# Performance work log

Measured on AMD Instinct MI355X. Metric: run time of the kernel, lower is better.

Reference implementation:

```python
import jax, jax.numpy as jnp
import numpy as np

N = 100000      # nodes
E = 1600000     # edges
F_IN = 64       # num_node_features
R = 8           # num_relations
G = 256         # graphs in batch
H, C = 4, 32    # GAT heads, per-head channels
NEG_SLOPE_ATT = 0.2    # GATConv attention leaky relu
NEG_SLOPE = 0.01       # F.leaky_relu default


def setup_inputs() -> dict:
    key = jax.random.key(0)
    ks = jax.random.split(key, 12)
    init = lambda k, shape, fan: (jax.random.normal(k, shape, jnp.float32) / np.sqrt(fan).astype(np.float32))
    x = jax.random.normal(ks[0], (N, F_IN), jnp.float32)
    edge_index = jax.random.randint(ks[1], (2, E), 0, N)
    edge_type = jax.random.randint(ks[2], (E,), 0, R)
    batch = (jnp.arange(N) * G) // N  # sorted graph ids, every segment non-empty
    return dict(
        x=x, edge_index=edge_index, edge_type=edge_type, batch=batch,
        gat_w=init(ks[3], (F_IN, H * C), F_IN),
        gat_att_src=init(ks[4], (H, C), C),
        gat_att_dst=init(ks[5], (H, C), C),
        gat_bias=jnp.zeros((H * C,), jnp.float32),
        dense1_w=init(ks[6], (H * C, 16), H * C),
        dense1_b=jnp.zeros((16,), jnp.float32),
        rw1=init(ks[7], (R, F_IN, 32), F_IN),
        root1=init(ks[8], (F_IN, 32), F_IN),
        rb1=jnp.zeros((32,), jnp.float32),
        rw2=init(ks[9], (R, 32, 16), 32),
        root2=init(ks[10], (32, 16), 32),
        rb2=jnp.zeros((16,), jnp.float32),
        dense_w=init(ks[11], (32, 1), 32),
        dense_b=jnp.zeros((1,), jnp.float32),
    )


def _gat(x, src, dst, w, att_src, att_dst, bias):
    h = (x @ w).reshape(N, H, C)                       # [N,H,C]
    a_src = jnp.sum(h * att_src, axis=-1)              # [N,H]
    a_dst = jnp.sum(h * att_dst, axis=-1)              # [N,H]
    e = jax.nn.leaky_relu(a_src[src] + a_dst[dst], NEG_SLOPE_ATT)  # [E,H]
    # segment softmax over incoming edges of each dst node
    m = jax.ops.segment_max(e, dst, num_segments=N)    # [N,H]
    p = jnp.exp(e - m[dst])
    s = jax.ops.segment_sum(p, dst, num_segments=N)    # [N,H]
    alpha = p / s[dst]
    msg = h[src] * alpha[:, :, None]                   # [E,H,C]
    out = jax.ops.segment_sum(msg, dst, num_segments=N)
    return out.reshape(N, H * C) + bias


def _rgcn(x, src, dst, edge_type, w, root, bias):
    # per-relation transform of all nodes, then edge gather (PyG RGCNConv, aggr='mean')
    xw = jnp.einsum('ni,rio->rno', x, w)               # [R,N,out]
    msg = xw[edge_type, src]                           # [E,out]
    comb = dst * R + edge_type                         # mean is per (dst, relation)
    cnt = jax.ops.segment_sum(jnp.ones((E,), x.dtype), comb, num_segments=N * R)
    agg = jax.ops.segment_sum(msg / cnt[comb][:, None], dst, num_segments=N)
    return agg + x @ root + bias


def reference(x, edge_index, edge_type, batch, gat_w, gat_att_src, gat_att_dst,
              gat_bias, dense1_w, dense1_b, rw1, root1, rb1, rw2, root2, rb2,
              dense_w, dense_b):
    src, dst = edge_index[0], edge_index[1]
    # GAT branch (dropout treated as identity / eval mode)
    h = _gat(x, src, dst, gat_w, gat_att_src, gat_att_dst, gat_bias)
    h = jax.nn.leaky_relu(h, NEG_SLOPE)
    h = jax.nn.leaky_relu(h @ dense1_w + dense1_b, NEG_SLOPE)
    gmax = jax.ops.segment_max(h, batch, num_segments=G)          # [G,16]
    # RGCN branch
    z = jax.nn.relu(_rgcn(x, src, dst, edge_type, rw1, root1, rb1))
    z = jax.nn.relu(_rgcn(z, src, dst, edge_type, rw2, root2, rb2))
    nodes_per_graph = jax.ops.segment_sum(jnp.ones((N,), x.dtype), batch, num_segments=G)
    gmean = jax.ops.segment_sum(z, batch, num_segments=G) / nodes_per_graph[:, None]
    # fuse
    zc = jnp.concatenate([gmax, gmean], axis=1)                   # [G,32]
    return zc @ dense_w + dense_b                                  # [G,1]
```

## Files before the change

### kernel.cpp

```cpp
#include <hip/hip_runtime.h>
#include <hip/hip_bf16.h>

typedef __hip_bfloat16 bf16;
typedef unsigned short u16;

#define N_NODES 100000
#define N_EDGES 1600000
#define F_IN 64
#define N_REL 8
#define N_GRAPH 256
#define N_HEAD 4
#define HC 128
#define NBLK_SCAN 391

__device__ __forceinline__ float lrelu(float x, float s) { return x >= 0.f ? x : s * x; }
__device__ __forceinline__ unsigned fenc(float f) {
  unsigned b = __float_as_uint(f);
  return (b & 0x80000000u) ? ~b : (b | 0x80000000u);
}
__device__ __forceinline__ float fdec(unsigned u) {
  float v = __uint_as_float((u & 0x80000000u) ? (u & 0x7fffffffu) : ~u);
  return fmaxf(fminf(v, 3e38f), -3e38f);
}
__device__ __forceinline__ float bf2f(bf16 v) { return __bfloat162float(v); }
__device__ __forceinline__ bf16 f2bf(float v) { return __float2bfloat16(v); }
__device__ __forceinline__ float lo_bf(unsigned u) { return __uint_as_float(u << 16); }
__device__ __forceinline__ float hi_bf(unsigned u) { return __uint_as_float(u & 0xFFFF0000u); }
__device__ __forceinline__ unsigned f2bfu(float v) {
  unsigned u = __float_as_uint(v);
  return (u + 0x7FFFu + ((u >> 16) & 1u)) >> 16;
}

template<bool BF> __device__ __forceinline__ float ldf(const void* p, size_t i) {
  if (BF) { u16 v = ((const u16*)p)[i]; return __uint_as_float(((unsigned)v) << 16); }
  else    { return ((const float*)p)[i]; }
}

__global__ void k_probe(const u16* __restrict__ xr, int* __restrict__ flag) {
  int t = threadIdx.x;
  int c = 0;
  for (int i = t; i < 1024; i += 256) {
    unsigned e = (xr[i] >> 7) & 0xFFu;
    if (e >= 100u && e <= 140u) c++;
  }
  __shared__ int sc[256];
  sc[t] = c;
  __syncthreads();
  for (int s = 128; s; s >>= 1) { if (t < s) sc[t] += sc[t + s]; __syncthreads(); }
  if (t == 0) *flag = (sc[0] >= 800) ? 1 : 0;
}

template<bool BF>
__device__ __forceinline__ void gat_h_body(const void* x, const void* w, const void* att_s,
                                           const void* att_d, u16* __restrict__ h,
                                           float* __restrict__ a_src, float* __restrict__ a_dst) {
  int n = blockIdx.x, j = threadIdx.x;
  __shared__ float xs[F_IN];
  if (j < F_IN) xs[j] = ldf<BF>(x, (size_t)n * F_IN + j);
  __syncthreads();
  float acc = 0.f;
#pragma unroll
  for (int k = 0; k < F_IN; ++k) acc += xs[k] * ldf<BF>(w, (size_t)k * HC + j);
  h[(size_t)n * HC + j] = (u16)f2bfu(acc);
  float ps = acc * ldf<BF>(att_s, j);
  float pd = acc * ldf<BF>(att_d, j);
#pragma unroll
  for (int off = 16; off > 0; off >>= 1) {
    ps += __shfl_down(ps, off, 32);
    pd += __shfl_down(pd, off, 32);
  }
  if ((j & 31) == 0) {
    a_src[n * N_HEAD + (j >> 5)] = ps;
    a_dst[n * N_HEAD + (j >> 5)] = pd;
  }
}
__global__ void k_gat_h(const void* x, const void* w, const void* att_s, const void* att_d,
                        u16* h, float* a_src, float* a_dst, const int* flag) {
  if (__builtin_amdgcn_readfirstlane(*flag)) gat_h_body<true>(x, w, att_s, att_d, h, a_src, a_dst);
  else gat_h_body<false>(x, w, att_s, att_d, h, a_src, a_dst);
}

__global__ void k_hist(const int* __restrict__ ei, const int* __restrict__ etype,
                       int* __restrict__ deg, int* __restrict__ cnt) {
  int e = blockIdx.x * 256 + threadIdx.x;
  if (e >= N_EDGES) return;
  int d = ei[N_EDGES + e], t = etype[e];
  atomicAdd(&deg[d], 1);
  atomicAdd(&cnt[d * N_REL + t], 1);
}

__global__ void k_scan_a(const int* __restrict__ deg, int* __restrict__ rowptr,
                         int* __restrict__ scanblk) {
  __shared__ int buf[256];
  int tid = threadIdx.x;
  int i = blockIdx.x * 256 + tid;
  int v = (i < N_NODES) ? deg[i] : 0;
  buf[tid] = v;
  __syncthreads();
  for (int st = 1; st < 256; st <<= 1) {
    int t = buf[tid];
    int a = (tid >= st) ? buf[tid - st] : 0;
    __syncthreads();
    buf[tid] = t + a;
    __syncthreads();
  }
  if (i < N_NODES) rowptr[i] = buf[tid] - v;
  if (tid == 255) scanblk[blockIdx.x] = buf[255];
}
__global__ void k_scan_b(int* __restrict__ scanblk) {
  __shared__ int buf[512];
  int tid = threadIdx.x;
  int v = (tid < NBLK_SCAN) ? scanblk[tid] : 0;
  buf[tid] = v;
  __syncthreads();
  for (int st = 1; st < 512; st <<= 1) {
    int t = buf[tid];
    int a = (tid >= st) ? buf[tid - st] : 0;
    __syncthreads();
    buf[tid] = t + a;
    __syncthreads();
  }
  if (tid < NBLK_SCAN) scanblk[tid] = buf[tid] - v;
}
__global__ void k_scan_c(int* __restrict__ rowptr, int* __restrict__ wp,
                         const int* __restrict__ scanblk) {
  int i = blockIdx.x * 256 + threadIdx.x;
  if (i < N_NODES) {
    int val = rowptr[i] + scanblk[blockIdx.x];
    rowptr[i] = val;
    wp[i] = val;
  } else if (i == N_NODES) {
    rowptr[N_NODES] = N_EDGES;
  }
}

__global__ void k_scatter(const int* __restrict__ ei, const int* __restrict__ etype,
                          const float* __restrict__ a_src, const float* __restrict__ a_dst,
                          int* __restrict__ wp, unsigned* __restrict__ csr,
                          float4* __restrict__ p_logit, int* __restrict__ dstarr) {
  int e = blockIdx.x * 256 + threadIdx.x;
  if (e >= N_EDGES) return;
  int sn = ei[e], d = ei[N_EDGES + e], t = etype[e];
  int pos = atomicAdd(&wp[d], 1);
  csr[pos] = (unsigned)sn | ((unsigned)t << 20);
  dstarr[pos] = d;
  const float4 as = *(const float4*)&a_src[sn * 4];
  const float4 ad = *(const float4*)&a_dst[d * 4];
  float4 lg;
  lg.x = lrelu(as.x + ad.x, 0.2f);
  lg.y = lrelu(as.y + ad.y, 0.2f);
  lg.z = lrelu(as.z + ad.z, 0.2f);
  lg.w = lrelu(as.w + ad.w, 0.2f);
  p_logit[pos] = lg;
}

__global__ void k_msum(const int* __restrict__ rowptr, const float* __restrict__ p_logit,
                       float* __restrict__ m_arr, float* __restrict__ si_arr) {
  int tid = threadIdx.x;
  int n = blockIdx.x * 16 + (tid >> 4);
  int l16 = tid & 15, head = l16 & 3, slot = l16 >> 2;
  int base = rowptr[n], deg = rowptr[n + 1] - base;
  float m = -1e30f;
  for (int i = slot; i < deg; i += 4) m = fmaxf(m, p_logit[(size_t)(base + i) * 4 + head]);
  m = fmaxf(m, __shfl_xor(m, 4, 64));
  m = fmaxf(m, __shfl_xor(m, 8, 64));
  float s = 0.f;
  for (int i = slot; i < deg; i += 4) s += __expf(p_logit[(size_t)(base + i) * 4 + head] - m);
  s += __shfl_xor(s, 4, 64);
  s += __shfl_xor(s, 8, 64);
  if (slot == 0) {
    m_arr[n * 4 + head] = m;
    si_arr[n * 4 + head] = (deg > 0) ? 1.f / s : 0.f;
  }
}

__global__ void k_alpha(const int* __restrict__ dstarr, const float* __restrict__ m_arr,
                        const float* __restrict__ si_arr, float4* __restrict__ plog4) {
  int p = blockIdx.x * 256 + threadIdx.x;
  if (p >= N_EDGES) return;
  int d = dstarr[p];
  float4 lg = plog4[p];
  const float4 m4 = *(const float4*)&m_arr[d * 4];
  const float4 s4 = *(const float4*)&si_arr[d * 4];
  float4 a;
  a.x = __expf(lg.x - m4.x) * s4.x;
  a.y = __expf(lg.y - m4.y) * s4.y;
  a.z = __expf(lg.z - m4.z) * s4.z;
  a.w = __expf(lg.w - m4.w) * s4.w;
  plog4[p] = a;
}

template<bool BF>
__device__ __forceinline__ void gat_agg_body(const int* __restrict__ rowptr,
                                             const unsigned* __restrict__ csr,
                                             const float* __restrict__ alpha,
                                             const uint2* __restrict__ hu2, const void* gbias,
                                             const void* d1w, const void* d1b,
                                             const int* __restrict__ batch,
                                             unsigned* __restrict__ gmax, int* __restrict__ npg) {
  int tid = threadIdx.x;
  int wave = tid >> 6, l = tid & 63;
  int d = blockIdx.x * 4 + wave;
  __shared__ float os[4][132];
  int base = rowptr[d];
  int deg = rowptr[d + 1] - base;
  int slot = l >> 5, cl = l & 31;
  int head = cl >> 3;
  float a0 = 0.f, a1 = 0.f, a2 = 0.f, a3 = 0.f;
  int i = slot;
  for (; i + 6 < deg; i += 8) {
    unsigned sp0 = csr[base + i],     sp1 = csr[base + i + 2];
    unsigned sp2 = csr[base + i + 4], sp3 = csr[base + i + 6];
    float av0 = alpha[(size_t)(base + i) * 4 + head];
    float av1 = alpha[(size_t)(base + i + 2) * 4 + head];
    float av2 = alpha[(size_t)(base + i + 4) * 4 + head];
    float av3 = alpha[(size_t)(base + i + 6) * 4 + head];
    uint2 h0 = hu2[(size_t)(sp0 & 0xFFFFF) * 32 + cl];
    uint2 h1 = hu2[(size_t)(sp1 & 0xFFFFF) * 32 + cl];
    uint2 h2 = hu2[(size_t)(sp2 & 0xFFFFF) * 32 + cl];
    uint2 h3 = hu2[(size_t)(sp3 & 0xFFFFF) * 32 + cl];
    a0 += lo_bf(h0.x) * av0 + lo_bf(h1.x) * av1 + lo_bf(h2.x) * av2 + lo_bf(h3.x) * av3;
    a1 += hi_bf(h0.x) * av0 + hi_bf(h1.x) * av1 + hi_bf(h2.x) * av2 + hi_bf(h3.x) * av3;
    a2 += lo_bf(h0.y) * av0 + lo_bf(h1.y) * av1 + lo_bf(h2.y) * av2 + lo_bf(h3.y) * av3;
    a3 += hi_bf(h0.y) * av0 + hi_bf(h1.y) * av1 + hi_bf(h2.y) * av2 + hi_bf(h3.y) * av3;
  }
  for (; i < deg; i += 2) {
    unsigned sp = csr[base + i];
    float av = alpha[(size_t)(base + i) * 4 + head];
    uint2 hv = hu2[(size_t)(sp & 0xFFFFF) * 32 + cl];
    a0 += lo_bf(hv.x) * av;
    a1 += hi_bf(hv.x) * av;
    a2 += lo_bf(hv.y) * av;
    a3 += hi_bf(hv.y) * av;
  }
  a0 += __shfl_xor(a0, 32, 64);
  a1 += __shfl_xor(a1, 32, 64);
  a2 += __shfl_xor(a2, 32, 64);
  a3 += __shfl_xor(a3, 32, 64);
  if (slot == 0) {
    os[wave][4 * cl + 0] = lrelu(a0 + ldf<BF>(gbias, 4 * cl + 0), 0.01f);
    os[wave][4 * cl + 1] = lrelu(a1 + ldf<BF>(gbias, 4 * cl + 1), 0.01f);
    os[wave][4 * cl + 2] = lrelu(a2 + ldf<BF>(gbias, 4 * cl + 2), 0.01f);
    os[wave][4 * cl + 3] = lrelu(a3 + ldf<BF>(gbias, 4 * cl + 3), 0.01f);
  }
  __syncthreads();
  if (tid < 64) {
    int node = tid >> 4, out = tid & 15;
    float acc = ldf<BF>(d1b, out);
#pragma unroll
    for (int k = 0; k < HC; ++k) acc += os[node][k] * ldf<BF>(d1w, (size_t)k * 16 + out);
    acc = lrelu(acc, 0.01f);
    atomicMax(&gmax[batch[blockIdx.x * 4 + node] * 16 + out], fenc(acc));
  }
  if (tid < 4) atomicAdd(&npg[batch[blockIdx.x * 4 + tid]], 1);
}
__global__ void k_gat_agg(const int* rowptr, const unsigned* csr, const float* alpha,
                          const u16* h, const void* gbias, const void* d1w, const void* d1b,
                          const int* batch, unsigned* gmax, int* npg, const int* flag) {
  if (__builtin_amdgcn_readfirstlane(*flag))
    gat_agg_body<true>(rowptr, csr, alpha, (const uint2*)h, gbias, d1w, d1b, batch, gmax, npg);
  else
    gat_agg_body<false>(rowptr, csr, alpha, (const uint2*)h, gbias, d1w, d1b, batch, gmax, npg);
}

template<bool BF>
__device__ __forceinline__ void xw1_body(const void* x, const void* rw1, bf16* __restrict__ xw1) {
  __shared__ float xs[8][F_IN];
  int tid = threadIdx.x;
  int n0 = blockIdx.x * 8;
  for (int i = tid; i < 8 * F_IN; i += 256) {
    int nn = n0 + (i >> 6);
    xs[i >> 6][i & 63] = (nn < N_NODES) ? ldf<BF>(x, (size_t)nn * F_IN + (i & 63)) : 0.f;
  }
  __syncthreads();
  int nl = tid >> 5, c = tid & 31;
  int n = n0 + nl, r = blockIdx.y;
  float acc = 0.f;
#pragma unroll
  for (int k = 0; k < F_IN; ++k) acc += xs[nl][k] * ldf<BF>(rw1, (size_t)(r * F_IN + k) * 32 + c);
  if (n < N_NODES) xw1[((size_t)r * N_NODES + n) * 32 + c] = f2bf(acc);
}
__global__ void k_xw1(const void* x, const void* rw1, bf16* xw1, const int* flag) {
  if (__builtin_amdgcn_readfirstlane(*flag)) xw1_body<true>(x, rw1, xw1);
  else xw1_body<false>(x, rw1, xw1);
}

template<bool BF>
__device__ __forceinline__ void ragg1_body(const int* __restrict__ rowptr,
                                           const unsigned* __restrict__ csr,
                                           const int* __restrict__ cnt,
                                           const u16* __restrict__ xw, const void* x,
                                           const void* root1, const void* rb1,
                                           float* __restrict__ z1) {
  __shared__ float xs[4][F_IN];
  __shared__ float cinv[4][N_REL];
  int tid = threadIdx.x;
  int n0 = blockIdx.x * 4;
  {
    int nn = n0 + (tid >> 6);
    xs[tid >> 6][tid & 63] = ldf<BF>(x, (size_t)nn * F_IN + (tid & 63));
  }
  if (tid < 32) {
    int cv = cnt[(n0 + (tid >> 3)) * N_REL + (tid & 7)];
    cinv[tid >> 3][tid & 7] = (cv > 0) ? 1.f / (float)cv : 0.f;
  }
  __syncthreads();
  int wave = tid >> 6, l = tid & 63;
  int half = l >> 5, c = l & 31;
  int n = n0 + wave;
  int base = rowptr[n], deg = rowptr[n + 1] - base;
  float acc = 0.f;
  int i = half;
  for (; i + 2 < deg; i += 4) {
    unsigned sp0 = csr[base + i], sp1 = csr[base + i + 2];
    int t0 = sp0 >> 20, t1 = sp1 >> 20;
    u16 v0 = xw[((size_t)t0 * N_NODES + (sp0 & 0xFFFFF)) * 32 + c];
    u16 v1 = xw[((size_t)t1 * N_NODES + (sp1 & 0xFFFFF)) * 32 + c];
    acc += __uint_as_float(((unsigned)v0) << 16) * cinv[wave][t0];
    acc += __uint_as_float(((unsigned)v1) << 16) * cinv[wave][t1];
  }
  if (i < deg) {
    unsigned sp = csr[base + i];
    int t = sp >> 20;
    u16 v = xw[((size_t)t * N_NODES + (sp & 0xFFFFF)) * 32 + c];
    acc += __uint_as_float(((unsigned)v) << 16) * cinv[wave][t];
  }
  float r = 0.f;
#pragma unroll
  for (int kk = 0; kk < 32; ++kk) {
    int k = half * 32 + kk;
    r += xs[wave][k] * ldf<BF>(root1, (size_t)k * 32 + c);
  }
  float tot = acc + r;
  tot += __shfl_xor(tot, 32, 64);
  if (half == 0) z1[(size_t)n * 32 + c] = fmaxf(tot + ldf<BF>(rb1, c), 0.f);
}
__global__ void k_ragg1(const int* rowptr, const unsigned* csr, const int* cnt,
                        const bf16* xw1, const void* x, const void* root1, const void* rb1,
                        float* z1, const int* flag) {
  if (__builtin_amdgcn_readfirstlane(*flag))
    ragg1_body<true>(rowptr, csr, cnt, (const u16*)xw1, x, root1, rb1, z1);
  else
    ragg1_body<false>(rowptr, csr, cnt, (const u16*)xw1, x, root1, rb1, z1);
}

template<bool BF>
__device__ __forceinline__ void zw2_body(const float* __restrict__ z1, const void* rw2,
                                         bf16* __restrict__ zw2) {
  __shared__ float zs[16][32];
  int tid = threadIdx.x;
  int n0 = blockIdx.x * 16;
  for (int i = tid; i < 16 * 32; i += 256) {
    int nn = n0 + (i >> 5);
    zs[i >> 5][i & 31] = (nn < N_NODES) ? z1[(size_t)nn * 32 + (i & 31)] : 0.f;
  }
  __syncthreads();
  int nl = tid >> 4, c = tid & 15;
  int n = n0 + nl, r = blockIdx.y;
  float acc = 0.f;
#pragma unroll
  for (int k = 0; k < 32; ++k) acc += zs[nl][k] * ldf<BF>(rw2, (size_t)(r * 32 + k) * 16 + c);
  if (n < N_NODES) zw2[((size_t)r * N_NODES + n) * 16 + c] = f2bf(acc);
}
__global__ void k_zw2(const float* z1, const void* rw2, bf16* zw2, const int* flag) {
  if (__builtin_amdgcn_readfirstlane(*flag)) zw2_body<true>(z1, rw2, zw2);
  else zw2_body<false>(z1, rw2, zw2);
}

template<bool BF>
__device__ __forceinline__ void ragg2_body(const int* __restrict__ rowptr,
                                           const unsigned* __restrict__ csr,
                                           const int* __restrict__ cnt,
                                           const u16* __restrict__ zw,
                                           const float* __restrict__ z1, const void* root2,
                                           const void* rb2, const int* __restrict__ batch,
                                           float* __restrict__ gsum) {
  __shared__ float zs[4][33];
  __shared__ float cinv[4][N_REL];
  int tid = threadIdx.x;
  int n0 = blockIdx.x * 4;
  if (tid < 128) {
    int nn = n0 + (tid >> 5);
    zs[tid >> 5][tid & 31] = z1[(size_t)nn * 32 + (tid & 31)];
  }
  if (tid < 32) {
    int cv = cnt[(n0 + (tid >> 3)) * N_REL + (tid & 7)];
    cinv[tid >> 3][tid & 7] = (cv > 0) ? 1.f / (float)cv : 0.f;
  }
  __syncthreads();
  int wave = tid >> 6, l = tid & 63;
  int q = l >> 4, c = l & 15;
  int n = n0 + wave;
  int base = rowptr[n], deg = rowptr[n + 1] - base;
  float acc = 0.f;
  int i = q;
  for (; i + 4 < deg; i += 8) {
    unsigned sp0 = csr[base + i], sp1 = csr[base + i + 4];
    int t0 = sp0 >> 20, t1 = sp1 >> 20;
    u16 v0 = zw[((size_t)t0 * N_NODES + (sp0 & 0xFFFFF)) * 16 + c];
    u16 v1 = zw[((size_t)t1 * N_NODES + (sp1 & 0xFFFFF)) * 16 + c];
    acc += __uint_as_float(((unsigned)v0) << 16) * cinv[wave][t0];
    acc += __uint_as_float(((unsigned)v1) << 16) * cinv[wave][t1];
  }
  if (i < deg) {
    unsigned sp = csr[base + i];
    int t = sp >> 20;
    u16 v = zw[((size_t)t * N_NODES + (sp & 0xFFFFF)) * 16 + c];
    acc += __uint_as_float(((unsigned)v) << 16) * cinv[wave][t];
  }
  float r = 0.f;
#pragma unroll
  for (int kk = 0; kk < 8; ++kk) {
    int k = q * 8 + kk;
    r += zs[wave][k] * ldf<BF>(root2, (size_t)k * 16 + c);
  }
  float tot = acc + r;
  tot += __shfl_xor(tot, 16, 64);
  tot += __shfl_xor(tot, 32, 64);
  if (q == 0) {
    float z2 = fmaxf(tot + ldf<BF>(rb2, c), 0.f);
    atomicAdd(&gsum[batch[n] * 16 + c], z2);
  }
}
__global__ void k_ragg2(const int* rowptr, const unsigned* csr, const int* cnt,
                        const bf16* zw2, const float* z1, const void* root2, const void* rb2,
                        const int* batch, float* gsum, const int* flag) {
  if (__builtin_amdgcn_readfirstlane(*flag))
    ragg2_body<true>(rowptr, csr, cnt, (const u16*)zw2, z1, root2, rb2, batch, gsum);
  else
    ragg2_body<false>(rowptr, csr, cnt, (const u16*)zw2, z1, root2, rb2, batch, gsum);
}

template<bool BF>
__device__ __forceinline__ void final_body(const unsigned* __restrict__ gmax,
                                           const float* __restrict__ gsum,
                                           const int* __restrict__ npg, const void* dw,
                                           const void* db, void* out) {
  int g = threadIdx.x;
  if (g >= N_GRAPH) return;
  float acc = ldf<BF>(db, 0);
  int np = npg[g]; if (np < 1) np = 1;
  float inv = 1.f / (float)np;
#pragma unroll
  for (int c = 0; c < 16; ++c) {
    acc += fdec(gmax[g * 16 + c]) * ldf<BF>(dw, c);
    acc += (gsum[g * 16 + c] * inv) * ldf<BF>(dw, 16 + c);
  }
  if (BF) ((bf16*)out)[g] = f2bf(acc);
  else ((float*)out)[g] = acc;
}
__global__ void k_final(const unsigned* gmax, const float* gsum, const int* npg,
                        const void* dw, const void* db, void* out, const int* flag) {
  if (__builtin_amdgcn_readfirstlane(*flag)) final_body<true>(gmax, gsum, npg, dw, db, out);
  else final_body<false>(gmax, gsum, npg, dw, db, out);
}

extern "C" void kernel_launch(void* const* d_in, const int* in_sizes, int n_in,
                              void* d_out, int out_size, void* d_ws, size_t ws_size,
                              hipStream_t stream) {
  const void* x        = d_in[0];
  const int*  ei       = (const int*)d_in[1];
  const int*  etype    = (const int*)d_in[2];
  const int*  batch    = (const int*)d_in[3];
  const void* gat_w    = d_in[4];
  const void* att_src  = d_in[5];
  const void* att_dst  = d_in[6];
  const void* gat_bias = d_in[7];
  const void* d1w      = d_in[8];
  const void* d1b      = d_in[9];
  const void* rw1      = d_in[10];
  const void* root1    = d_in[11];
  const void* rb1      = d_in[12];
  const void* rw2      = d_in[13];
  const void* root2    = d_in[14];
  const void* rb2      = d_in[15];
  const void* dw       = d_in[16];
  const void* db       = d_in[17];

  char* ws = (char*)d_ws;
  const size_t o_h     = 0;
  const size_t o_plog  = 25600000;
  const size_t o_xw1   = 0;
  const size_t o_zw2   = 0;
  const size_t o_asrc  = 51200000;
  const size_t o_adst  = 52800000;
  const size_t o_deg   = 54400000;
  const size_t o_rowp  = 54800000;
  const size_t o_wp    = 55200016;
  const size_t o_cnt   = 55600032;
  const size_t o_csr   = 58800032;
  const size_t o_z1    = 65200032;
  const size_t o_sblk  = 78000032;
  const size_t o_gmax  = 78001600;
  const size_t o_gsum  = 78017984;
  const size_t o_npg   = 78034368;
  const size_t o_flag  = 78035392;
  const size_t o_dst   = 78035400;
  const size_t total   = 84435400;
  if (ws_size < total) return;

  u16*      h      = (u16*)(ws + o_h);
  float*    plog   = (float*)(ws + o_plog);
  bf16*     xw1    = (bf16*)(ws + o_xw1);
  bf16*     zw2    = (bf16*)(ws + o_zw2);
  float*    a_src  = (float*)(ws + o_asrc);
  float*    a_dst  = (float*)(ws + o_adst);
  int*      deg    = (int*)(ws + o_deg);
  int*      rowptr = (int*)(ws + o_rowp);
  int*      wp     = (int*)(ws + o_wp);
  int*      cnt    = (int*)(ws + o_cnt);
  unsigned* csr    = (unsigned*)(ws + o_csr);
  float*    z1     = (float*)(ws + o_z1);
  int*      sblk   = (int*)(ws + o_sblk);
  unsigned* gmax   = (unsigned*)(ws + o_gmax);
  float*    gsum   = (float*)(ws + o_gsum);
  int*      npg    = (int*)(ws + o_npg);
  int*      flag   = (int*)(ws + o_flag);
  int*      dstarr = (int*)(ws + o_dst);

  k_probe<<<1, 256, 0, stream>>>((const u16*)x, flag);

  hipMemsetAsync(ws + o_deg, 0, o_csr - o_deg, stream);
  hipMemsetAsync(ws + o_gmax, 0, 33792, stream);

  k_gat_h<<<N_NODES, 128, 0, stream>>>(x, gat_w, att_src, att_dst, h, a_src, a_dst, flag);

  k_hist<<<(N_EDGES + 255) / 256, 256, 0, stream>>>(ei, etype, deg, cnt);
  k_scan_a<<<NBLK_SCAN, 256, 0, stream>>>(deg, rowptr, sblk);
  k_scan_b<<<1, 512, 0, stream>>>(sblk);
  k_scan_c<<<NBLK_SCAN, 256, 0, stream>>>(rowptr, wp, sblk);
  k_scatter<<<(N_EDGES + 255) / 256, 256, 0, stream>>>(ei, etype, a_src, a_dst, wp, csr,
                                                       (float4*)plog, dstarr);

  k_msum<<<N_NODES / 16, 256, 0, stream>>>(rowptr, plog, a_src, a_dst);
  k_alpha<<<(N_EDGES + 255) / 256, 256, 0, stream>>>(dstarr, a_src, a_dst, (float4*)plog);

  k_gat_agg<<<N_NODES / 4, 256, 0, stream>>>(rowptr, csr, plog, h, gat_bias, d1w, d1b, batch,
                                             gmax, npg, flag);

  k_xw1<<<dim3((N_NODES + 7) / 8, N_REL), 256, 0, stream>>>(x, rw1, xw1, flag);
  k_ragg1<<<N_NODES / 4, 256, 0, stream>>>(rowptr, csr, cnt, xw1, x, root1, rb1, z1, flag);

  k_zw2<<<dim3((N_NODES + 15) / 16, N_REL), 256, 0, stream>>>(z1, rw2, zw2, flag);
  k_ragg2<<<N_NODES / 4, 256, 0, stream>>>(rowptr, csr, cnt, zw2, z1, root2, rb2,
                                           batch, gsum, flag);

  k_final<<<1, 256, 0, stream>>>(gmax, gsum, npg, dw, db, d_out, flag);
}
```

Measured before the change: 1.231 ms.

## Aggregate raw features per relation before transform, fuse GAT projection with histogram

RGCN layers no longer precompute per-relation transformed features (xw1, zw2) for all nodes. Instead each destination node sums raw bf16 neighbour features per relation in registers and then applies the relation weights once per node, using the linearity of the mean aggregation. This removes two large precompute kernels and their scattered gathers, at the cost of an 8-way per-relation accumulator, more registers, and a small per-node matmul. The GAT projection kernel and the degree histogram are merged into one launch, and bf16 copies of x and z1 are written for the gathers.

```diff
diff --git a/kernel.cpp b/kernel.cpp
--- a/kernel.cpp
+++ b/kernel.cpp
@@ -22,10 +22,9 @@
   float v = __uint_as_float((u & 0x80000000u) ? (u & 0x7fffffffu) : ~u);
   return fmaxf(fminf(v, 3e38f), -3e38f);
 }
-__device__ __forceinline__ float bf2f(bf16 v) { return __bfloat162float(v); }
-__device__ __forceinline__ bf16 f2bf(float v) { return __float2bfloat16(v); }
 __device__ __forceinline__ float lo_bf(unsigned u) { return __uint_as_float(u << 16); }
 __device__ __forceinline__ float hi_bf(unsigned u) { return __uint_as_float(u & 0xFFFF0000u); }
+__device__ __forceinline__ bf16 f2bf(float v) { return __float2bfloat16(v); }
 __device__ __forceinline__ unsigned f2bfu(float v) {
   unsigned u = __float_as_uint(v);
   return (u + 0x7FFFu + ((u >> 16) & 1u)) >> 16;
@@ -53,11 +52,13 @@
 template<bool BF>
 __device__ __forceinline__ void gat_h_body(const void* x, const void* w, const void* att_s,
                                            const void* att_d, u16* __restrict__ h,
-                                           float* __restrict__ a_src, float* __restrict__ a_dst) {
-  int n = blockIdx.x, j = threadIdx.x;
-  __shared__ float xs[F_IN];
+                                           u16* __restrict__ xb,
+                                           float* __restrict__ a_src, float* __restrict__ a_dst,
+                                           int n, float* xs) {
+  int j = threadIdx.x;
   if (j < F_IN) xs[j] = ldf<BF>(x, (size_t)n * F_IN + j);
   __syncthreads();
+  if (!BF && j < F_IN) xb[(size_t)n * F_IN + j] = (u16)f2bfu(xs[j]);
   float acc = 0.f;
 #pragma unroll
   for (int k = 0; k < F_IN; ++k) acc += xs[k] * ldf<BF>(w, (size_t)k * HC + j);
@@ -74,19 +75,25 @@
     a_dst[n * N_HEAD + (j >> 5)] = pd;
   }
 }
-__global__ void k_gat_h(const void* x, const void* w, const void* att_s, const void* att_d,
-                        u16* h, float* a_src, float* a_dst, const int* flag) {
-  if (__builtin_amdgcn_readfirstlane(*flag)) gat_h_body<true>(x, w, att_s, att_d, h, a_src, a_dst);
-  else gat_h_body<false>(x, w, att_s, att_d, h, a_src, a_dst);
-}
-
-__global__ void k_hist(const int* __restrict__ ei, const int* __restrict__ etype,
-                       int* __restrict__ deg, int* __restrict__ cnt) {
-  int e = blockIdx.x * 256 + threadIdx.x;
-  if (e >= N_EDGES) return;
-  int d = ei[N_EDGES + e], t = etype[e];
-  atomicAdd(&deg[d], 1);
-  atomicAdd(&cnt[d * N_REL + t], 1);
+
+__global__ void k_gath_hist(const void* x, const void* w, const void* att_s, const void* att_d,
+                            u16* h, u16* xb, float* a_src, float* a_dst,
+                            const int* __restrict__ ei, const int* __restrict__ etype,
+                            int* __restrict__ deg, int* __restrict__ cnt, const int* flag) {
+  __shared__ float xs[F_IN];
+  if (blockIdx.x < N_NODES) {
+    if (__builtin_amdgcn_readfirstlane(*flag))
+      gat_h_body<true>(x, w, att_s, att_d, h, xb, a_src, a_dst, blockIdx.x, xs);
+    else
+      gat_h_body<false>(x, w, att_s, att_d, h, xb, a_src, a_dst, blockIdx.x, xs);
+  } else {
+    int e = (blockIdx.x - N_NODES) * 128 + threadIdx.x;
+    if (e < N_EDGES) {
+      int d = ei[N_EDGES + e], t = etype[e];
+      atomicAdd(&deg[d], 1);
+      atomicAdd(&cnt[d * N_REL + t], 1);
+    }
+  }
 }
 
 __global__ void k_scan_a(const int* __restrict__ deg, int* __restrict__ rowptr,
@@ -197,11 +204,11 @@
                                              const uint2* __restrict__ hu2, const void* gbias,
                                              const void* d1w, const void* d1b,
                                              const int* __restrict__ batch,
-                                             unsigned* __restrict__ gmax, int* __restrict__ npg) {
+                                             unsigned* __restrict__ gmax, int* __restrict__ npg,
+                                             float (*os)[132]) {
   int tid = threadIdx.x;
   int wave = tid >> 6, l = tid & 63;
   int d = blockIdx.x * 4 + wave;
-  __shared__ float os[4][132];
   int base = rowptr[d];
   int deg = rowptr[d + 1] - base;
   int slot = l >> 5, cl = l & 31;
@@ -257,178 +264,214 @@
 __global__ void k_gat_agg(const int* rowptr, const unsigned* csr, const float* alpha,
                           const u16* h, const void* gbias, const void* d1w, const void* d1b,
                           const int* batch, unsigned* gmax, int* npg, const int* flag) {
+  __shared__ float os[4][132];
   if (__builtin_amdgcn_readfirstlane(*flag))
-    gat_agg_body<true>(rowptr, csr, alpha, (const uint2*)h, gbias, d1w, d1b, batch, gmax, npg);
+    gat_agg_body<true>(rowptr, csr, alpha, (const uint2*)h, gbias, d1w, d1b, batch, gmax, npg, os);
   else
-    gat_agg_body<false>(rowptr, csr, alpha, (const uint2*)h, gbias, d1w, d1b, batch, gmax, npg);
-}
-
-template<bool BF>
-__device__ __forceinline__ void xw1_body(const void* x, const void* rw1, bf16* __restrict__ xw1) {
-  __shared__ float xs[8][F_IN];
-  int tid = threadIdx.x;
-  int n0 = blockIdx.x * 8;
-  for (int i = tid; i < 8 * F_IN; i += 256) {
-    int nn = n0 + (i >> 6);
-    xs[i >> 6][i & 63] = (nn < N_NODES) ? ldf<BF>(x, (size_t)nn * F_IN + (i & 63)) : 0.f;
-  }
-  __syncthreads();
-  int nl = tid >> 5, c = tid & 31;
-  int n = n0 + nl, r = blockIdx.y;
-  float acc = 0.f;
-#pragma unroll
-  for (int k = 0; k < F_IN; ++k) acc += xs[nl][k] * ldf<BF>(rw1, (size_t)(r * F_IN + k) * 32 + c);
-  if (n < N_NODES) xw1[((size_t)r * N_NODES + n) * 32 + c] = f2bf(acc);
-}
-__global__ void k_xw1(const void* x, const void* rw1, bf16* xw1, const int* flag) {
-  if (__builtin_amdgcn_readfirstlane(*flag)) xw1_body<true>(x, rw1, xw1);
-  else xw1_body<false>(x, rw1, xw1);
+    gat_agg_body<false>(rowptr, csr, alpha, (const uint2*)h, gbias, d1w, d1b, batch, gmax, npg, os);
 }
 
 template<bool BF>
 __device__ __forceinline__ void ragg1_body(const int* __restrict__ rowptr,
                                            const unsigned* __restrict__ csr,
                                            const int* __restrict__ cnt,
-                                           const u16* __restrict__ xw, const void* x,
-                                           const void* root1, const void* rb1,
-                                           float* __restrict__ z1) {
-  __shared__ float xs[4][F_IN];
-  __shared__ float cinv[4][N_REL];
+                                           const unsigned* __restrict__ xbu, const void* x,
+                                           const void* rw1, const void* root1, const void* rb1,
+                                           float* __restrict__ z1, u16* __restrict__ z1b,
+                                           float (*sacc)[N_REL][F_IN], float (*cinv)[N_REL]) {
   int tid = threadIdx.x;
   int n0 = blockIdx.x * 4;
-  {
-    int nn = n0 + (tid >> 6);
-    xs[tid >> 6][tid & 63] = ldf<BF>(x, (size_t)nn * F_IN + (tid & 63));
-  }
+  for (int i = tid; i < 4 * N_REL * F_IN; i += 256) ((float*)sacc)[i] = 0.f;
   if (tid < 32) {
     int cv = cnt[(n0 + (tid >> 3)) * N_REL + (tid & 7)];
     cinv[tid >> 3][tid & 7] = (cv > 0) ? 1.f / (float)cv : 0.f;
   }
   __syncthreads();
   int wave = tid >> 6, l = tid & 63;
-  int half = l >> 5, c = l & 31;
+  int slot = l >> 5, cl = l & 31;
   int n = n0 + wave;
   int base = rowptr[n], deg = rowptr[n + 1] - base;
-  float acc = 0.f;
-  int i = half;
+  float acc[N_REL][2];
+#pragma unroll
+  for (int r = 0; r < N_REL; ++r) { acc[r][0] = 0.f; acc[r][1] = 0.f; }
+  int i = slot;
   for (; i + 2 < deg; i += 4) {
     unsigned sp0 = csr[base + i], sp1 = csr[base + i + 2];
+    unsigned v0 = xbu[(size_t)(sp0 & 0xFFFFF) * 32 + cl];
+    unsigned v1 = xbu[(size_t)(sp1 & 0xFFFFF) * 32 + cl];
     int t0 = sp0 >> 20, t1 = sp1 >> 20;
-    u16 v0 = xw[((size_t)t0 * N_NODES + (sp0 & 0xFFFFF)) * 32 + c];
-    u16 v1 = xw[((size_t)t1 * N_NODES + (sp1 & 0xFFFFF)) * 32 + c];
-    acc += __uint_as_float(((unsigned)v0) << 16) * cinv[wave][t0];
-    acc += __uint_as_float(((unsigned)v1) << 16) * cinv[wave][t1];
+    float l0 = lo_bf(v0), h0 = hi_bf(v0), l1 = lo_bf(v1), h1 = hi_bf(v1);
+#pragma unroll
+    for (int r = 0; r < N_REL; ++r) {
+      acc[r][0] += (t0 == r ? l0 : 0.f) + (t1 == r ? l1 : 0.f);
+      acc[r][1] += (t0 == r ? h0 : 0.f) + (t1 == r ? h1 : 0.f);
+    }
   }
   if (i < deg) {
     unsigned sp = csr[base + i];
+    unsigned v = xbu[(size_t)(sp & 0xFFFFF) * 32 + cl];
     int t = sp >> 20;
-    u16 v = xw[((size_t)t * N_NODES + (sp & 0xFFFFF)) * 32 + c];
-    acc += __uint_as_float(((unsigned)v) << 16) * cinv[wave][t];
-  }
-  float r = 0.f;
-#pragma unroll
-  for (int kk = 0; kk < 32; ++kk) {
-    int k = half * 32 + kk;
-    r += xs[wave][k] * ldf<BF>(root1, (size_t)k * 32 + c);
-  }
-  float tot = acc + r;
-  tot += __shfl_xor(tot, 32, 64);
-  if (half == 0) z1[(size_t)n * 32 + c] = fmaxf(tot + ldf<BF>(rb1, c), 0.f);
+    float lv = lo_bf(v), hv = hi_bf(v);
+#pragma unroll
+    for (int r = 0; r < N_REL; ++r) {
+      acc[r][0] += (t == r ? lv : 0.f);
+      acc[r][1] += (t == r ? hv : 0.f);
+    }
+  }
+#pragma unroll
+  for (int r = 0; r < N_REL; ++r) {
+    acc[r][0] += __shfl_xor(acc[r][0], 32, 64);
+    acc[r][1] += __shfl_xor(acc[r][1], 32, 64);
+  }
+  if (slot == 0) {
+#pragma unroll
+    for (int r = 0; r < N_REL; ++r) {
+      sacc[wave][r][2 * cl]     = acc[r][0];
+      sacc[wave][r][2 * cl + 1] = acc[r][1];
+    }
+  }
+  __syncthreads();
+  {
+    int c = l & 31, half = l >> 5;
+    float a = 0.f;
+#pragma unroll
+    for (int r = 0; r < N_REL; ++r) {
+      float ci = cinv[wave][r];
+      float pr = 0.f;
+#pragma unroll
+      for (int kk = 0; kk < 32; ++kk) {
+        int k = half * 32 + kk;
+        pr += sacc[wave][r][k] * ldf<BF>(rw1, (size_t)(r * F_IN + k) * 32 + c);
+      }
+      a += ci * pr;
+    }
+#pragma unroll
+    for (int kk = 0; kk < 32; ++kk) {
+      int k = half * 32 + kk;
+      a += ldf<BF>(x, (size_t)n * F_IN + k) * ldf<BF>(root1, (size_t)k * 32 + c);
+    }
+    a += __shfl_xor(a, 32, 64);
+    if (half == 0) {
+      float zv = fmaxf(a + ldf<BF>(rb1, c), 0.f);
+      z1[(size_t)n * 32 + c] = zv;
+      z1b[(size_t)n * 32 + c] = (u16)f2bfu(zv);
+    }
+  }
 }
 __global__ void k_ragg1(const int* rowptr, const unsigned* csr, const int* cnt,
-                        const bf16* xw1, const void* x, const void* root1, const void* rb1,
-                        float* z1, const int* flag) {
+                        const u16* xb, const void* x, const void* rw1, const void* root1,
+                        const void* rb1, float* z1, u16* z1b, const int* flag) {
+  __shared__ float sacc[4][N_REL][F_IN];
+  __shared__ float cinv[4][N_REL];
   if (__builtin_amdgcn_readfirstlane(*flag))
-    ragg1_body<true>(rowptr, csr, cnt, (const u16*)xw1, x, root1, rb1, z1);
+    ragg1_body<true>(rowptr, csr, cnt, (const unsigned*)x, x, rw1, root1, rb1, z1, z1b,
+                     sacc, cinv);
   else
-    ragg1_body<false>(rowptr, csr, cnt, (const u16*)xw1, x, root1, rb1, z1);
-}
-
-template<bool BF>
-__device__ __forceinline__ void zw2_body(const float* __restrict__ z1, const void* rw2,
-                                         bf16* __restrict__ zw2) {
-  __shared__ float zs[16][32];
-  int tid = threadIdx.x;
-  int n0 = blockIdx.x * 16;
-  for (int i = tid; i < 16 * 32; i += 256) {
-    int nn = n0 + (i >> 5);
-    zs[i >> 5][i & 31] = (nn < N_NODES) ? z1[(size_t)nn * 32 + (i & 31)] : 0.f;
-  }
-  __syncthreads();
-  int nl = tid >> 4, c = tid & 15;
-  int n = n0 + nl, r = blockIdx.y;
-  float acc = 0.f;
-#pragma unroll
-  for (int k = 0; k < 32; ++k) acc += zs[nl][k] * ldf<BF>(rw2, (size_t)(r * 32 + k) * 16 + c);
-  if (n < N_NODES) zw2[((size_t)r * N_NODES + n) * 16 + c] = f2bf(acc);
-}
-__global__ void k_zw2(const float* z1, const void* rw2, bf16* zw2, const int* flag) {
-  if (__builtin_amdgcn_readfirstlane(*flag)) zw2_body<true>(z1, rw2, zw2);
-  else zw2_body<false>(z1, rw2, zw2);
+    ragg1_body<false>(rowptr, csr, cnt, (const unsigned*)xb, x, rw1, root1, rb1, z1, z1b,
+                      sacc, cinv);
 }
 
 template<bool BF>
 __device__ __forceinline__ void ragg2_body(const int* __restrict__ rowptr,
                                            const unsigned* __restrict__ csr,
                                            const int* __restrict__ cnt,
-                                           const u16* __restrict__ zw,
-                                           const float* __restrict__ z1, const void* root2,
-                                           const void* rb2, const int* __restrict__ batch,
-                                           float* __restrict__ gsum) {
-  __shared__ float zs[4][33];
-  __shared__ float cinv[4][N_REL];
+                                           const unsigned* __restrict__ zbu,
+                                           const float* __restrict__ z1,
+                                           const void* rw2, const void* root2, const void* rb2,
+                                           const int* __restrict__ batch,
+                                           float* __restrict__ gsum,
+                                           float (*sacc)[N_REL][32], float (*cinv)[N_REL]) {
   int tid = threadIdx.x;
   int n0 = blockIdx.x * 4;
-  if (tid < 128) {
-    int nn = n0 + (tid >> 5);
-    zs[tid >> 5][tid & 31] = z1[(size_t)nn * 32 + (tid & 31)];
-  }
+  for (int i = tid; i < 4 * N_REL * 32; i += 256) ((float*)sacc)[i] = 0.f;
   if (tid < 32) {
     int cv = cnt[(n0 + (tid >> 3)) * N_REL + (tid & 7)];
     cinv[tid >> 3][tid & 7] = (cv > 0) ? 1.f / (float)cv : 0.f;
   }
   __syncthreads();
   int wave = tid >> 6, l = tid & 63;
-  int q = l >> 4, c = l & 15;
+  int slot = l >> 4, cl = l & 15;
   int n = n0 + wave;
   int base = rowptr[n], deg = rowptr[n + 1] - base;
-  float acc = 0.f;
-  int i = q;
+  float acc[N_REL][2];
+#pragma unroll
+  for (int r = 0; r < N_REL; ++r) { acc[r][0] = 0.f; acc[r][1] = 0.f; }
+  int i = slot;
   for (; i + 4 < deg; i += 8) {
     unsigned sp0 = csr[base + i], sp1 = csr[base + i + 4];
+    unsigned v0 = zbu[(size_t)(sp0 & 0xFFFFF) * 16 + cl];
+    unsigned v1 = zbu[(size_t)(sp1 & 0xFFFFF) * 16 + cl];
     int t0 = sp0 >> 20, t1 = sp1 >> 20;
-    u16 v0 = zw[((size_t)t0 * N_NODES + (sp0 & 0xFFFFF)) * 16 + c];
-    u16 v1 = zw[((size_t)t1 * N_NODES + (sp1 & 0xFFFFF)) * 16 + c];
-    acc += __uint_as_float(((unsigned)v0) << 16) * cinv[wave][t0];
-    acc += __uint_as_float(((unsigned)v1) << 16) * cinv[wave][t1];
+    float l0 = lo_bf(v0), h0 = hi_bf(v0), l1 = lo_bf(v1), h1 = hi_bf(v1);
+#pragma unroll
+    for (int r = 0; r < N_REL; ++r) {
+      acc[r][0] += (t0 == r ? l0 : 0.f) + (t1 == r ? l1 : 0.f);
+      acc[r][1] += (t0 == r ? h0 : 0.f) + (t1 == r ? h1 : 0.f);
+    }
   }
   if (i < deg) {
     unsigned sp = csr[base + i];
+    unsigned v = zbu[(size_t)(sp & 0xFFFFF) * 16 + cl];
     int t = sp >> 20;
-    u16 v = zw[((size_t)t * N_NODES + (sp & 0xFFFFF)) * 16 + c];
-    acc += __uint_as_float(((unsigned)v) << 16) * cinv[wave][t];
-  }
-  float r = 0.f;
-#pragma unroll
-  for (int kk = 0; kk < 8; ++kk) {
-    int k = q * 8 + kk;
-    r += zs[wave][k] * ldf<BF>(root2, (size_t)k * 16 + c);
-  }
-  float tot = acc + r;
-  tot += __shfl_xor(tot, 16, 64);
-  tot += __shfl_xor(tot, 32, 64);
-  if (q == 0) {
-    float z2 = fmaxf(tot + ldf<BF>(rb2, c), 0.f);
-    atomicAdd(&gsum[batch[n] * 16 + c], z2);
+    float lv = lo_bf(v), hv = hi_bf(v);
+#pragma unroll
+    for (int r = 0; r < N_REL; ++r) {
+      acc[r][0] += (t == r ? lv : 0.f);
+      acc[r][1] += (t == r ? hv : 0.f);
+    }
+  }
+#pragma unroll
+  for (int r = 0; r < N_REL; ++r) {
+    acc[r][0] += __shfl_xor(acc[r][0], 16, 64);
+    acc[r][0] += __shfl_xor(acc[r][0], 32, 64);
+    acc[r][1] += __shfl_xor(acc[r][1], 16, 64);
+    acc[r][1] += __shfl_xor(acc[r][1], 32, 64);
+  }
+  if (slot == 0) {
+#pragma unroll
+    for (int r = 0; r < N_REL; ++r) {
+      sacc[wave][r][2 * cl]     = acc[r][0];
+      sacc[wave][r][2 * cl + 1] = acc[r][1];
+    }
+  }
+  __syncthreads();
+  {
+    int c = l & 15, q = l >> 4;
+    float a = 0.f;
+#pragma unroll
+    for (int rr = 0; rr < 2; ++rr) {
+      int r = q * 2 + rr;
+      float ci = cinv[wave][r];
+      float pr = 0.f;
+#pragma unroll
+      for (int k = 0; k < 32; ++k)
+        pr += sacc[wave][r][k] * ldf<BF>(rw2, (size_t)(r * 32 + k) * 16 + c);
+      a += ci * pr;
+    }
+#pragma unroll
+    for (int kk = 0; kk < 8; ++kk) {
+      int k = q * 8 + kk;
+      a += z1[(size_t)n * 32 + k] * ldf<BF>(root2, (size_t)k * 16 + c);
+    }
+    a += __shfl_xor(a, 16, 64);
+    a += __shfl_xor(a, 32, 64);
+    if (q == 0) {
+      float z2 = fmaxf(a + ldf<BF>(rb2, c), 0.f);
+      atomicAdd(&gsum[batch[n] * 16 + c], z2);
+    }
   }
 }
 __global__ void k_ragg2(const int* rowptr, const unsigned* csr, const int* cnt,
-                        const bf16* zw2, const float* z1, const void* root2, const void* rb2,
-                        const int* batch, float* gsum, const int* flag) {
+                        const u16* z1b, const float* z1, const void* rw2, const void* root2,
+                        const void* rb2, const int* batch, float* gsum, const int* flag) {
+  __shared__ float sacc[4][N_REL][32];
+  __shared__ float cinv[4][N_REL];
   if (__builtin_amdgcn_readfirstlane(*flag))
-    ragg2_body<true>(rowptr, csr, cnt, (const u16*)zw2, z1, root2, rb2, batch, gsum);
+    ragg2_body<true>(rowptr, csr, cnt, (const unsigned*)z1b, z1, rw2, root2, rb2, batch,
+                     gsum, sacc, cinv);
   else
-    ragg2_body<false>(rowptr, csr, cnt, (const u16*)zw2, z1, root2, rb2, batch, gsum);
+    ragg2_body<false>(rowptr, csr, cnt, (const unsigned*)z1b, z1, rw2, root2, rb2, batch,
+                      gsum, sacc, cinv);
 }
 
 template<bool BF>
@@ -480,29 +523,30 @@
   char* ws = (char*)d_ws;
   const size_t o_h     = 0;
   const size_t o_plog  = 25600000;
-  const size_t o_xw1   = 0;
-  const size_t o_zw2   = 0;
-  const size_t o_asrc  = 51200000;
-  const size_t o_adst  = 52800000;
-  const size_t o_deg   = 54400000;
-  const size_t o_rowp  = 54800000;
-  const size_t o_wp    = 55200016;
-  const size_t o_cnt   = 55600032;
-  const size_t o_csr   = 58800032;
-  const size_t o_z1    = 65200032;
-  const size_t o_sblk  = 78000032;
-  const size_t o_gmax  = 78001600;
-  const size_t o_gsum  = 78017984;
-  const size_t o_npg   = 78034368;
-  const size_t o_flag  = 78035392;
-  const size_t o_dst   = 78035400;
-  const size_t total   = 84435400;
+  const size_t o_xb    = 51200000;
+  const size_t o_z1b   = 64000000;
+  const size_t o_dst   = 70400000;
+  const size_t o_asrc  = 76800000;
+  const size_t o_adst  = 78400000;
+  const size_t o_deg   = 80000000;
+  const size_t o_rowp  = 80400000;
+  const size_t o_wp    = 80800016;
+  const size_t o_cnt   = 81200032;
+  const size_t o_csr   = 84400032;
+  const size_t o_z1    = 90800032;
+  const size_t o_sblk  = 103600032;
+  const size_t o_gmax  = 103601600;
+  const size_t o_gsum  = 103617984;
+  const size_t o_npg   = 103634368;
+  const size_t o_flag  = 103635392;
+  const size_t total   = 103635396;
   if (ws_size < total) return;
 
   u16*      h      = (u16*)(ws + o_h);
   float*    plog   = (float*)(ws + o_plog);
-  bf16*     xw1    = (bf16*)(ws + o_xw1);
-  bf16*     zw2    = (bf16*)(ws + o_zw2);
+  u16*      xb     = (u16*)(ws + o_xb);
+  u16*      z1b    = (u16*)(ws + o_z1b);
+  int*      dstarr = (int*)(ws + o_dst);
   float*    a_src  = (float*)(ws + o_asrc);
   float*    a_dst  = (float*)(ws + o_adst);
   int*      deg    = (int*)(ws + o_deg);
@@ -516,16 +560,15 @@
   float*    gsum   = (float*)(ws + o_gsum);
   int*      npg    = (int*)(ws + o_npg);
   int*      flag   = (int*)(ws + o_flag);
-  int*      dstarr = (int*)(ws + o_dst);
 
   k_probe<<<1, 256, 0, stream>>>((const u16*)x, flag);
 
   hipMemsetAsync(ws + o_deg, 0, o_csr - o_deg, stream);
   hipMemsetAsync(ws + o_gmax, 0, 33792, stream);
 
-  k_gat_h<<<N_NODES, 128, 0, stream>>>(x, gat_w, att_src, att_dst, h, a_src, a_dst, flag);
-
-  k_hist<<<(N_EDGES + 255) / 256, 256, 0, stream>>>(ei, etype, deg, cnt);
+  k_gath_hist<<<N_NODES + 12500, 128, 0, stream>>>(x, gat_w, att_src, att_dst, h, xb,
+                                                   a_src, a_dst, ei, etype, deg, cnt, flag);
+
   k_scan_a<<<NBLK_SCAN, 256, 0, stream>>>(deg, rowptr, sblk);
   k_scan_b<<<1, 512, 0, stream>>>(sblk);
   k_scan_c<<<NBLK_SCAN, 256, 0, stream>>>(rowptr, wp, sblk);
@@ -535,14 +578,13 @@
   k_msum<<<N_NODES / 16, 256, 0, stream>>>(rowptr, plog, a_src, a_dst);
   k_alpha<<<(N_EDGES + 255) / 256, 256, 0, stream>>>(dstarr, a_src, a_dst, (float4*)plog);
 
-  k_gat_agg<<<N_NODES / 4, 256, 0, stream>>>(rowptr, csr, plog, h, gat_bias, d1w, d1b, batch,
-                                             gmax, npg, flag);
-
-  k_xw1<<<dim3((N_NODES + 7) / 8, N_REL), 256, 0, stream>>>(x, rw1, xw1, flag);
-  k_ragg1<<<N_NODES / 4, 256, 0, stream>>>(rowptr, csr, cnt, xw1, x, root1, rb1, z1, flag);
-
-  k_zw2<<<dim3((N_NODES + 15) / 16, N_REL), 256, 0, stream>>>(z1, rw2, zw2, flag);
-  k_ragg2<<<N_NODES / 4, 256, 0, stream>>>(rowptr, csr, cnt, zw2, z1, root2, rb2,
+  k_gat_agg<<<N_NODES / 4, 256, 0, stream>>>(rowptr, csr, plog, h, gat_bias, d1w, d1b,
+                                             batch, gmax, npg, flag);
+
+  k_ragg1<<<N_NODES / 4, 256, 0, stream>>>(rowptr, csr, cnt, xb, x, rw1, root1, rb1,
+                                           z1, z1b, flag);
+
+  k_ragg2<<<N_NODES / 4, 256, 0, stream>>>(rowptr, csr, cnt, z1b, z1, rw2, root2, rb2,
                                            batch, gsum, flag);
 
   k_final<<<1, 256, 0, stream>>>(gmax, gsum, npg, dw, db, d_out, flag);
```

Result: slower. 1.296 ms (+5.2%).
